# Optimization experiments

Measured on AMD Instinct MI355X. Metric: run time of the kernel, lower is better.

Reference implementation:

```python
import jax, jax.numpy as jnp
import numpy as np


def setup_inputs() -> dict:
    key = jax.random.key(0)
    k1, k2, k3 = jax.random.split(key, 3)
    Na, Nb, D, K = 1024, 1024, 512, 256
    a = jax.random.normal(k1, (Na, D), dtype=jnp.float32)
    b = jax.random.normal(k2, (Nb, D), dtype=jnp.float32)
    feats = jax.random.normal(k3, (K, D), dtype=jnp.float32)
    return {"a": a, "b": b, "feats": feats}


def reference(a, b, feats):
    # 'ignorematch' mode of the Difference module.
    # Project both sets onto the feature bank: [Na,K] and [Nb,K]
    a_fk = jnp.matmul(a, feats.T)          # [Na, K]
    b_fk = jnp.matmul(b, feats.T)          # [Nb, K]
    a_e = a_fk[:, None, :]                 # [Na, 1, K]
    b_e = b_fk[None, :, :]                 # [1, Nb, K]
    # features present in a (>0) but absent in b (<=0)
    mask = ((a_e > 0) & (b_e <= 0)).astype(a_fk.dtype)  # [Na, Nb, K]
    result = jnp.sum(a_e * mask, axis=2)   # [Na, Nb]
    return result
```

## Files before the change

kernel.cpp:

```cpp
#include <hip/hip_runtime.h>
#include <hip/hip_bf16.h>


typedef short bf16x8 __attribute__((ext_vector_type(8)));
typedef float f32x4  __attribute__((ext_vector_type(4)));

__device__ inline void split3(float x, __hip_bfloat16& h, __hip_bfloat16& m, __hip_bfloat16& l) {
    h = __float2bfloat16(x);
    float r1 = x - __bfloat162float(h);
    m = __float2bfloat16(r1);
    float r2 = r1 - __bfloat162float(m);
    l = __float2bfloat16(r2);
}

__global__ __launch_bounds__(256) void convert_kernel(
    const float* __restrict__ a, const float* __restrict__ b, const float* __restrict__ f,
    __hip_bfloat16* __restrict__ Ah, __hip_bfloat16* __restrict__ Am,
    __hip_bfloat16* __restrict__ Bh, __hip_bfloat16* __restrict__ Bm, __hip_bfloat16* __restrict__ Bl,
    __hip_bfloat16* __restrict__ Fh, __hip_bfloat16* __restrict__ Fm, __hip_bfloat16* __restrict__ Fl)
{
    const int t = blockIdx.x * 256 + threadIdx.x;
    const int i4 = t * 4;

    {
        float4 v = *(const float4*)(a + i4);
        __hip_bfloat16 h[4] __attribute__((aligned(8)));
        __hip_bfloat16 m[4] __attribute__((aligned(8)));
        __hip_bfloat16 l;
        split3(v.x, h[0], m[0], l); split3(v.y, h[1], m[1], l);
        split3(v.z, h[2], m[2], l); split3(v.w, h[3], m[3], l);
        *(short4*)((short*)Ah + i4) = *(const short4*)h;
        *(short4*)((short*)Am + i4) = *(const short4*)m;
    }
    {
        float4 v = *(const float4*)(b + i4);
        __hip_bfloat16 h[4] __attribute__((aligned(8)));
        __hip_bfloat16 m[4] __attribute__((aligned(8)));
        __hip_bfloat16 l[4] __attribute__((aligned(8)));
        split3(v.x, h[0], m[0], l[0]); split3(v.y, h[1], m[1], l[1]);
        split3(v.z, h[2], m[2], l[2]); split3(v.w, h[3], m[3], l[3]);
        *(short4*)((short*)Bh + i4) = *(const short4*)h;
        *(short4*)((short*)Bm + i4) = *(const short4*)m;
        *(short4*)((short*)Bl + i4) = *(const short4*)l;
    }
    {
        float x = f[t];
        __hip_bfloat16 h, m, l;
        split3(x, h, m, l);
        Fh[t] = h; Fm[t] = m; Fl[t] = l;
    }
}

__global__ __launch_bounds__(256) void stage1_kernel(
    const __hip_bfloat16* __restrict__ Ah, const __hip_bfloat16* __restrict__ Am,
    const __hip_bfloat16* __restrict__ Bh, const __hip_bfloat16* __restrict__ Bm,
    const __hip_bfloat16* __restrict__ Bl,
    const __hip_bfloat16* __restrict__ Fh, const __hip_bfloat16* __restrict__ Fm,
    const __hip_bfloat16* __restrict__ Fl,
    __hip_bfloat16* __restrict__ pbf, __hip_bfloat16* __restrict__ mbf)
{
    const int idx = blockIdx.x;
    const bool isA = idx < 256;
    const int t  = idx & 255;
    const int bi = t >> 3;
    const int bn = t & 7;
    const int m0 = bi * 32;
    const int n0 = bn * 32;

    const int tid  = threadIdx.x;
    const int w    = tid >> 6;
    const int lane = tid & 63;
    const int wi = w >> 1, wj = w & 1;
    const int l15 = lane & 15;
    const int q   = lane >> 4;

    const int ra = (m0 + wi * 16 + l15) * 512;
    const int rf = (n0 + wj * 16 + l15) * 512;

    f32x4 acc = {0.f, 0.f, 0.f, 0.f};

    if (isA) {
        const short* ah_p = (const short*)Ah + ra;
        const short* am_p = (const short*)Am + ra;
        const short* fh_p = (const short*)Fh + rf;
        const short* fm_p = (const short*)Fm + rf;
        #pragma unroll 4
        for (int k0 = 0; k0 < 512; k0 += 32) {
            const int ko = k0 + q * 8;
            bf16x8 ah = *(const bf16x8*)(ah_p + ko);
            bf16x8 am = *(const bf16x8*)(am_p + ko);
            bf16x8 fh = *(const bf16x8*)(fh_p + ko);
            bf16x8 fm = *(const bf16x8*)(fm_p + ko);
            acc = __builtin_amdgcn_mfma_f32_16x16x32_bf16(ah, fh, acc, 0, 0, 0);
            acc = __builtin_amdgcn_mfma_f32_16x16x32_bf16(ah, fm, acc, 0, 0, 0);
            acc = __builtin_amdgcn_mfma_f32_16x16x32_bf16(am, fh, acc, 0, 0, 0);
        }
        const int orow = m0 + wi * 16 + q * 4;
        const int ocol = n0 + wj * 16 + l15;
        #pragma unroll
        for (int r = 0; r < 4; r++)
            pbf[(size_t)(orow + r) * 256 + ocol] = __float2bfloat16(fmaxf(acc[r], 0.f));
    } else {
        const short* bh_p = (const short*)Bh + ra;
        const short* bm_p = (const short*)Bm + ra;
        const short* bl_p = (const short*)Bl + ra;
        const short* fh_p = (const short*)Fh + rf;
        const short* fm_p = (const short*)Fm + rf;
        const short* fl_p = (const short*)Fl + rf;
        #pragma unroll 4
        for (int k0 = 0; k0 < 512; k0 += 32) {
            const int ko = k0 + q * 8;
            bf16x8 bh = *(const bf16x8*)(bh_p + ko);
            bf16x8 bm = *(const bf16x8*)(bm_p + ko);
            bf16x8 bl = *(const bf16x8*)(bl_p + ko);
            bf16x8 fh = *(const bf16x8*)(fh_p + ko);
            bf16x8 fm = *(const bf16x8*)(fm_p + ko);
            bf16x8 fl = *(const bf16x8*)(fl_p + ko);
            acc = __builtin_amdgcn_mfma_f32_16x16x32_bf16(bh, fh, acc, 0, 0, 0);
            acc = __builtin_amdgcn_mfma_f32_16x16x32_bf16(bh, fm, acc, 0, 0, 0);
            acc = __builtin_amdgcn_mfma_f32_16x16x32_bf16(bm, fh, acc, 0, 0, 0);
            acc = __builtin_amdgcn_mfma_f32_16x16x32_bf16(bh, fl, acc, 0, 0, 0);
            acc = __builtin_amdgcn_mfma_f32_16x16x32_bf16(bl, fh, acc, 0, 0, 0);
            acc = __builtin_amdgcn_mfma_f32_16x16x32_bf16(bm, fm, acc, 0, 0, 0);
        }
        const int orow = m0 + wi * 16 + q * 4;
        const int ocol = n0 + wj * 16 + l15;
        #pragma unroll
        for (int r = 0; r < 4; r++)
            mbf[(size_t)(orow + r) * 256 + ocol] = __float2bfloat16(acc[r] <= 0.f ? 1.f : 0.f);
    }
}

__global__ __launch_bounds__(256) void gemm2_kernel(
    const __hip_bfloat16* __restrict__ p, const __hip_bfloat16* __restrict__ m,
    float* __restrict__ out)
{
    const int bi = blockIdx.x >> 4;
    const int bj = blockIdx.x & 15;
    const int i0 = bi * 32;
    const int j0 = bj * 64;

    const int tid  = threadIdx.x;
    const int w    = tid >> 6;
    const int lane = tid & 63;
    const int wi = w >> 1, wj = w & 1;
    const int l15 = lane & 15;
    const int q   = lane >> 4;

    const int arow  = i0 + wi * 16 + l15;
    const int jbase = j0 + wj * 32;
    const int brow0 = jbase + l15;
    const int brow1 = brow0 + 16;

    const short* ps = (const short*)p;
    const short* ms = (const short*)m;

    f32x4 acc0 = {0.f, 0.f, 0.f, 0.f};
    f32x4 acc1 = {0.f, 0.f, 0.f, 0.f};

    #pragma unroll
    for (int k0 = 0; k0 < 256; k0 += 32) {
        const int ko = k0 + q * 8;
        bf16x8 av = *(const bf16x8*)(ps + (size_t)arow  * 256 + ko);
        bf16x8 b0 = *(const bf16x8*)(ms + (size_t)brow0 * 256 + ko);
        bf16x8 b1 = *(const bf16x8*)(ms + (size_t)brow1 * 256 + ko);
        acc0 = __builtin_amdgcn_mfma_f32_16x16x32_bf16(av, b0, acc0, 0, 0, 0);
        acc1 = __builtin_amdgcn_mfma_f32_16x16x32_bf16(av, b1, acc1, 0, 0, 0);
    }

    const int orow = i0 + wi * 16 + q * 4;
    const int ocol = jbase + l15;
    #pragma unroll
    for (int r = 0; r < 4; r++) {
        out[(size_t)(orow + r) * 1024 + ocol]      = acc0[r];
        out[(size_t)(orow + r) * 1024 + ocol + 16] = acc1[r];
    }
}

extern "C" void kernel_launch(void* const* d_in, const int* in_sizes, int n_in,
                              void* d_out, int out_size, void* d_ws, size_t ws_size,
                              hipStream_t stream) {
    const float* a     = (const float*)d_in[0];
    const float* b     = (const float*)d_in[1];
    const float* feats = (const float*)d_in[2];
    float* out = (float*)d_out;

    const size_t NAB = 1024 * 512;
    const size_t NF  = 256 * 512;
    __hip_bfloat16* w0 = (__hip_bfloat16*)d_ws;
    __hip_bfloat16* Ah = w0;
    __hip_bfloat16* Am = Ah + NAB;
    __hip_bfloat16* Bh = Am + NAB;
    __hip_bfloat16* Bm = Bh + NAB;
    __hip_bfloat16* Bl = Bm + NAB;
    __hip_bfloat16* Fh = Bl + NAB;
    __hip_bfloat16* Fm = Fh + NF;
    __hip_bfloat16* Fl = Fm + NF;
    __hip_bfloat16* pbf = Fl + NF;
    __hip_bfloat16* mbf = pbf + 1024 * 256;

    convert_kernel<<<512, 256, 0, stream>>>(a, b, feats, Ah, Am, Bh, Bm, Bl, Fh, Fm, Fl);
    stage1_kernel <<<512, 256, 0, stream>>>(Ah, Am, Bh, Bm, Bl, Fh, Fm, Fl, pbf, mbf);
    gemm2_kernel  <<<512, 256, 0, stream>>>(pbf, mbf, out);
}
```

Before: 88.34 us.

## Fuse three kernels into one persistent kernel with grid barriers

Merges the convert, stage-1 projection and final GEMM kernels into a single 256-block kernel that uses atomic-counter grid barriers between phases, with a memset to reset the barrier counters. Stage 1 now computes the A and B projections in the same block using two accumulators, and the final GEMM uses 64x64 tiles per block. The goal is to remove launch gaps between kernels. In exchange it adds barrier spin overhead and a memset launch, and it relies on all 256 blocks being co-resident so the spin barrier cannot deadlock.

```diff
diff --git a/kernel.cpp b/kernel.cpp
--- a/kernel.cpp
+++ b/kernel.cpp
@@ -13,16 +13,35 @@
     l = __float2bfloat16(r2);
 }
 
-__global__ __launch_bounds__(256) void convert_kernel(
+__device__ inline void grid_barrier(unsigned* cnt, unsigned* flag, int nblk) {
+    __syncthreads();
+    if (threadIdx.x == 0) {
+        __threadfence();
+        if (atomicAdd(cnt, 1u) == (unsigned)(nblk - 1)) {
+            atomicExch(flag, 1u);
+        } else {
+            while (atomicAdd(flag, 0u) == 0u) { __builtin_amdgcn_s_sleep(1); }
+        }
+        __threadfence();
+    }
+    __syncthreads();
+}
+
+__global__ __launch_bounds__(256) void fused_kernel(
     const float* __restrict__ a, const float* __restrict__ b, const float* __restrict__ f,
+    unsigned* __restrict__ bar,
     __hip_bfloat16* __restrict__ Ah, __hip_bfloat16* __restrict__ Am,
     __hip_bfloat16* __restrict__ Bh, __hip_bfloat16* __restrict__ Bm, __hip_bfloat16* __restrict__ Bl,
-    __hip_bfloat16* __restrict__ Fh, __hip_bfloat16* __restrict__ Fm, __hip_bfloat16* __restrict__ Fl)
+    __hip_bfloat16* __restrict__ Fh, __hip_bfloat16* __restrict__ Fm, __hip_bfloat16* __restrict__ Fl,
+    __hip_bfloat16* __restrict__ pbf, __hip_bfloat16* __restrict__ mbf,
+    float* __restrict__ out)
 {
-    const int t = blockIdx.x * 256 + threadIdx.x;
-    const int i4 = t * 4;
-
-    {
+    const int tid = threadIdx.x;
+    const int t   = blockIdx.x * 256 + tid;
+
+    #pragma unroll
+    for (int r = 0; r < 2; r++) {
+        int i4 = (t + r * 65536) * 4;
         float4 v = *(const float4*)(a + i4);
         __hip_bfloat16 h[4] __attribute__((aligned(8)));
         __hip_bfloat16 m[4] __attribute__((aligned(8)));
@@ -32,7 +51,9 @@
         *(short4*)((short*)Ah + i4) = *(const short4*)h;
         *(short4*)((short*)Am + i4) = *(const short4*)m;
     }
-    {
+    #pragma unroll
+    for (int r = 0; r < 2; r++) {
+        int i4 = (t + r * 65536) * 4;
         float4 v = *(const float4*)(b + i4);
         __hip_bfloat16 h[4] __attribute__((aligned(8)));
         __hip_bfloat16 m[4] __attribute__((aligned(8)));
@@ -43,137 +64,112 @@
         *(short4*)((short*)Bm + i4) = *(const short4*)m;
         *(short4*)((short*)Bl + i4) = *(const short4*)l;
     }
+    if (t < 32768) {
+        int i4 = t * 4;
+        float4 v = *(const float4*)(f + i4);
+        __hip_bfloat16 h[4] __attribute__((aligned(8)));
+        __hip_bfloat16 m[4] __attribute__((aligned(8)));
+        __hip_bfloat16 l[4] __attribute__((aligned(8)));
+        split3(v.x, h[0], m[0], l[0]); split3(v.y, h[1], m[1], l[1]);
+        split3(v.z, h[2], m[2], l[2]); split3(v.w, h[3], m[3], l[3]);
+        *(short4*)((short*)Fh + i4) = *(const short4*)h;
+        *(short4*)((short*)Fm + i4) = *(const short4*)m;
+        *(short4*)((short*)Fl + i4) = *(const short4*)l;
+    }
+
+    grid_barrier(bar + 0, bar + 1, gridDim.x);
+
     {
-        float x = f[t];
-        __hip_bfloat16 h, m, l;
-        split3(x, h, m, l);
-        Fh[t] = h; Fm[t] = m; Fl[t] = l;
-    }
-}
-
-__global__ __launch_bounds__(256) void stage1_kernel(
-    const __hip_bfloat16* __restrict__ Ah, const __hip_bfloat16* __restrict__ Am,
-    const __hip_bfloat16* __restrict__ Bh, const __hip_bfloat16* __restrict__ Bm,
-    const __hip_bfloat16* __restrict__ Bl,
-    const __hip_bfloat16* __restrict__ Fh, const __hip_bfloat16* __restrict__ Fm,
-    const __hip_bfloat16* __restrict__ Fl,
-    __hip_bfloat16* __restrict__ pbf, __hip_bfloat16* __restrict__ mbf)
-{
-    const int idx = blockIdx.x;
-    const bool isA = idx < 256;
-    const int t  = idx & 255;
-    const int bi = t >> 3;
-    const int bn = t & 7;
-    const int m0 = bi * 32;
-    const int n0 = bn * 32;
-
-    const int tid  = threadIdx.x;
-    const int w    = tid >> 6;
-    const int lane = tid & 63;
-    const int wi = w >> 1, wj = w & 1;
-    const int l15 = lane & 15;
-    const int q   = lane >> 4;
-
-    const int ra = (m0 + wi * 16 + l15) * 512;
-    const int rf = (n0 + wj * 16 + l15) * 512;
-
-    f32x4 acc = {0.f, 0.f, 0.f, 0.f};
-
-    if (isA) {
+        const int jb = blockIdx.x;
+        const int m0 = (jb >> 3) * 32;
+        const int n0 = (jb & 7) * 32;
+        const int w  = tid >> 6;
+        const int lane = tid & 63;
+        const int wi = w >> 1, wj = w & 1;
+        const int l15 = lane & 15;
+        const int q   = lane >> 4;
+
+        const int ra = (m0 + wi * 16 + l15) * 512;
+        const int rf = (n0 + wj * 16 + l15) * 512;
         const short* ah_p = (const short*)Ah + ra;
         const short* am_p = (const short*)Am + ra;
-        const short* fh_p = (const short*)Fh + rf;
-        const short* fm_p = (const short*)Fm + rf;
-        #pragma unroll 4
-        for (int k0 = 0; k0 < 512; k0 += 32) {
-            const int ko = k0 + q * 8;
-            bf16x8 ah = *(const bf16x8*)(ah_p + ko);
-            bf16x8 am = *(const bf16x8*)(am_p + ko);
-            bf16x8 fh = *(const bf16x8*)(fh_p + ko);
-            bf16x8 fm = *(const bf16x8*)(fm_p + ko);
-            acc = __builtin_amdgcn_mfma_f32_16x16x32_bf16(ah, fh, acc, 0, 0, 0);
-            acc = __builtin_amdgcn_mfma_f32_16x16x32_bf16(ah, fm, acc, 0, 0, 0);
-            acc = __builtin_amdgcn_mfma_f32_16x16x32_bf16(am, fh, acc, 0, 0, 0);
-        }
-        const int orow = m0 + wi * 16 + q * 4;
-        const int ocol = n0 + wj * 16 + l15;
-        #pragma unroll
-        for (int r = 0; r < 4; r++)
-            pbf[(size_t)(orow + r) * 256 + ocol] = __float2bfloat16(fmaxf(acc[r], 0.f));
-    } else {
         const short* bh_p = (const short*)Bh + ra;
         const short* bm_p = (const short*)Bm + ra;
         const short* bl_p = (const short*)Bl + ra;
         const short* fh_p = (const short*)Fh + rf;
         const short* fm_p = (const short*)Fm + rf;
         const short* fl_p = (const short*)Fl + rf;
+
+        f32x4 accA = {0.f, 0.f, 0.f, 0.f};
+        f32x4 accB = {0.f, 0.f, 0.f, 0.f};
+
         #pragma unroll 4
         for (int k0 = 0; k0 < 512; k0 += 32) {
             const int ko = k0 + q * 8;
+            bf16x8 ah = *(const bf16x8*)(ah_p + ko);
+            bf16x8 am = *(const bf16x8*)(am_p + ko);
             bf16x8 bh = *(const bf16x8*)(bh_p + ko);
             bf16x8 bm = *(const bf16x8*)(bm_p + ko);
             bf16x8 bl = *(const bf16x8*)(bl_p + ko);
             bf16x8 fh = *(const bf16x8*)(fh_p + ko);
             bf16x8 fm = *(const bf16x8*)(fm_p + ko);
             bf16x8 fl = *(const bf16x8*)(fl_p + ko);
-            acc = __builtin_amdgcn_mfma_f32_16x16x32_bf16(bh, fh, acc, 0, 0, 0);
-            acc = __builtin_amdgcn_mfma_f32_16x16x32_bf16(bh, fm, acc, 0, 0, 0);
-            acc = __builtin_amdgcn_mfma_f32_16x16x32_bf16(bm, fh, acc, 0, 0, 0);
-            acc = __builtin_amdgcn_mfma_f32_16x16x32_bf16(bh, fl, acc, 0, 0, 0);
-            acc = __builtin_amdgcn_mfma_f32_16x16x32_bf16(bl, fh, acc, 0, 0, 0);
-            acc = __builtin_amdgcn_mfma_f32_16x16x32_bf16(bm, fm, acc, 0, 0, 0);
-        }
+            accA = __builtin_amdgcn_mfma_f32_16x16x32_bf16(ah, fh, accA, 0, 0, 0);
+            accB = __builtin_amdgcn_mfma_f32_16x16x32_bf16(bh, fh, accB, 0, 0, 0);
+            accA = __builtin_amdgcn_mfma_f32_16x16x32_bf16(ah, fm, accA, 0, 0, 0);
+            accB = __builtin_amdgcn_mfma_f32_16x16x32_bf16(bh, fm, accB, 0, 0, 0);
+            accA = __builtin_amdgcn_mfma_f32_16x16x32_bf16(am, fh, accA, 0, 0, 0);
+            accB = __builtin_amdgcn_mfma_f32_16x16x32_bf16(bm, fh, accB, 0, 0, 0);
+            accB = __builtin_amdgcn_mfma_f32_16x16x32_bf16(bh, fl, accB, 0, 0, 0);
+            accB = __builtin_amdgcn_mfma_f32_16x16x32_bf16(bl, fh, accB, 0, 0, 0);
+            accB = __builtin_amdgcn_mfma_f32_16x16x32_bf16(bm, fm, accB, 0, 0, 0);
+        }
+
         const int orow = m0 + wi * 16 + q * 4;
         const int ocol = n0 + wj * 16 + l15;
         #pragma unroll
-        for (int r = 0; r < 4; r++)
-            mbf[(size_t)(orow + r) * 256 + ocol] = __float2bfloat16(acc[r] <= 0.f ? 1.f : 0.f);
-    }
-}
-
-__global__ __launch_bounds__(256) void gemm2_kernel(
-    const __hip_bfloat16* __restrict__ p, const __hip_bfloat16* __restrict__ m,
-    float* __restrict__ out)
-{
-    const int bi = blockIdx.x >> 4;
-    const int bj = blockIdx.x & 15;
-    const int i0 = bi * 32;
-    const int j0 = bj * 64;
-
-    const int tid  = threadIdx.x;
-    const int w    = tid >> 6;
-    const int lane = tid & 63;
-    const int wi = w >> 1, wj = w & 1;
-    const int l15 = lane & 15;
-    const int q   = lane >> 4;
-
-    const int arow  = i0 + wi * 16 + l15;
-    const int jbase = j0 + wj * 32;
-    const int brow0 = jbase + l15;
-    const int brow1 = brow0 + 16;
-
-    const short* ps = (const short*)p;
-    const short* ms = (const short*)m;
-
-    f32x4 acc0 = {0.f, 0.f, 0.f, 0.f};
-    f32x4 acc1 = {0.f, 0.f, 0.f, 0.f};
-
-    #pragma unroll
-    for (int k0 = 0; k0 < 256; k0 += 32) {
-        const int ko = k0 + q * 8;
-        bf16x8 av = *(const bf16x8*)(ps + (size_t)arow  * 256 + ko);
-        bf16x8 b0 = *(const bf16x8*)(ms + (size_t)brow0 * 256 + ko);
-        bf16x8 b1 = *(const bf16x8*)(ms + (size_t)brow1 * 256 + ko);
-        acc0 = __builtin_amdgcn_mfma_f32_16x16x32_bf16(av, b0, acc0, 0, 0, 0);
-        acc1 = __builtin_amdgcn_mfma_f32_16x16x32_bf16(av, b1, acc1, 0, 0, 0);
-    }
-
-    const int orow = i0 + wi * 16 + q * 4;
-    const int ocol = jbase + l15;
-    #pragma unroll
-    for (int r = 0; r < 4; r++) {
-        out[(size_t)(orow + r) * 1024 + ocol]      = acc0[r];
-        out[(size_t)(orow + r) * 1024 + ocol + 16] = acc1[r];
+        for (int r = 0; r < 4; r++) {
+            pbf[(size_t)(orow + r) * 256 + ocol] = __float2bfloat16(fmaxf(accA[r], 0.f));
+            mbf[(size_t)(orow + r) * 256 + ocol] = __float2bfloat16(accB[r] <= 0.f ? 1.f : 0.f);
+        }
+    }
+
+    grid_barrier(bar + 2, bar + 3, gridDim.x);
+
+    {
+        const int i0 = (blockIdx.x >> 4) * 64;
+        const int j0 = (blockIdx.x & 15) * 64;
+        const int w  = tid >> 6;
+        const int lane = tid & 63;
+        const int l15 = lane & 15;
+        const int q   = lane >> 4;
+
+        const int arow = i0 + w * 16 + l15;
+        const short* ps = (const short*)pbf + (size_t)arow * 256;
+        const short* ms = (const short*)mbf;
+
+        f32x4 acc[4];
+        #pragma unroll
+        for (int c = 0; c < 4; c++) acc[c] = (f32x4){0.f, 0.f, 0.f, 0.f};
+
+        #pragma unroll
+        for (int k0 = 0; k0 < 256; k0 += 32) {
+            const int ko = k0 + q * 8;
+            bf16x8 av = *(const bf16x8*)(ps + ko);
+            #pragma unroll
+            for (int c = 0; c < 4; c++) {
+                bf16x8 bv = *(const bf16x8*)(ms + (size_t)(j0 + c * 16 + l15) * 256 + ko);
+                acc[c] = __builtin_amdgcn_mfma_f32_16x16x32_bf16(av, bv, acc[c], 0, 0, 0);
+            }
+        }
+
+        const int orow = i0 + w * 16 + q * 4;
+        const int ocol = j0 + l15;
+        #pragma unroll
+        for (int c = 0; c < 4; c++)
+            #pragma unroll
+            for (int r = 0; r < 4; r++)
+                out[(size_t)(orow + r) * 1024 + ocol + c * 16] = acc[c][r];
     }
 }
 
@@ -185,21 +181,22 @@
     const float* feats = (const float*)d_in[2];
     float* out = (float*)d_out;
 
-    const size_t NAB = 1024 * 512;
-    const size_t NF  = 256 * 512;
-    __hip_bfloat16* w0 = (__hip_bfloat16*)d_ws;
-    __hip_bfloat16* Ah = w0;
-    __hip_bfloat16* Am = Ah + NAB;
-    __hip_bfloat16* Bh = Am + NAB;
-    __hip_bfloat16* Bm = Bh + NAB;
-    __hip_bfloat16* Bl = Bm + NAB;
-    __hip_bfloat16* Fh = Bl + NAB;
-    __hip_bfloat16* Fm = Fh + NF;
-    __hip_bfloat16* Fl = Fm + NF;
-    __hip_bfloat16* pbf = Fl + NF;
-    __hip_bfloat16* mbf = pbf + 1024 * 256;
-
-    convert_kernel<<<512, 256, 0, stream>>>(a, b, feats, Ah, Am, Bh, Bm, Bl, Fh, Fm, Fl);
-    stage1_kernel <<<512, 256, 0, stream>>>(Ah, Am, Bh, Bm, Bl, Fh, Fm, Fl, pbf, mbf);
-    gemm2_kernel  <<<512, 256, 0, stream>>>(pbf, mbf, out);
-}
+    char* base = (char*)d_ws;
+    unsigned* bar = (unsigned*)base;
+    const size_t MB = 1024 * 1024;
+    __hip_bfloat16* Ah  = (__hip_bfloat16*)(base + 1024);
+    __hip_bfloat16* Am  = (__hip_bfloat16*)(base + 1024 + 1 * MB);
+    __hip_bfloat16* Bh  = (__hip_bfloat16*)(base + 1024 + 2 * MB);
+    __hip_bfloat16* Bm  = (__hip_bfloat16*)(base + 1024 + 3 * MB);
+    __hip_bfloat16* Bl  = (__hip_bfloat16*)(base + 1024 + 4 * MB);
+    __hip_bfloat16* Fh  = (__hip_bfloat16*)(base + 1024 + 5 * MB);
+    __hip_bfloat16* Fm  = (__hip_bfloat16*)(base + 1024 + 5 * MB + 256 * 1024);
+    __hip_bfloat16* Fl  = (__hip_bfloat16*)(base + 1024 + 5 * MB + 512 * 1024);
+    __hip_bfloat16* pbf = (__hip_bfloat16*)(base + 1024 + 6 * MB);
+    __hip_bfloat16* mbf = (__hip_bfloat16*)(base + 1024 + 6 * MB + 512 * 1024);
+
+    hipMemsetAsync(bar, 0, 64, stream);
+    fused_kernel<<<256, 256, 0, stream>>>(a, b, feats, bar,
+                                          Ah, Am, Bh, Bm, Bl, Fh, Fm, Fl,
+                                          pbf, mbf, out);
+}
```

Result: slower. 130.8 us (+48.0%).
